# Kernel optimization log

Measured on AMD Instinct MI355X. Metric: run time of the kernel, lower is better.

## Reference

```python
import jax, jax.numpy as jnp
import numpy as np

B, L, T, H = 8, 16, 1024, 256


def setup_inputs() -> dict:
    key = jax.random.key(0)
    k1, k2 = jax.random.split(key)
    h_blth = jax.random.normal(k1, (B, L, T, H), dtype=jnp.float32)
    # nn.Linear(H, 1): weight [1, H] -> store as [H]; bias [1]
    attn_w = jax.random.normal(k2, (H,), dtype=jnp.float32) / np.sqrt(H)
    attn_b = jnp.zeros((1,), dtype=jnp.float32)
    return {"h_blth": h_blth, "attn_w": attn_w, "attn_b": attn_b}


def reference(h_blth, attn_w, attn_b):
    # scores: [B, L, T]
    s = jnp.einsum('blth,h->blt', h_blth, attn_w) + attn_b[0]
    # global max over T (matches torch .max(dim=2, keepdim=True))
    s_max = jnp.max(s, axis=2, keepdims=True)
    exp_s = jnp.exp(s - s_max)                      # [B, L, T]
    cum_exp = jnp.cumsum(exp_s, axis=2)             # [B, L, T]
    weighted_h = exp_s[..., None] * h_blth          # [B, L, T, H]
    cum_weighted_h = jnp.cumsum(weighted_h, axis=2) # [B, L, T, H]
    ctx = cum_weighted_h / (cum_exp[..., None] + 1e-12)
    return h_blth + ctx
```

## Files before the change

kernel.cpp:

```cpp
#include <hip/hip_runtime.h>


constexpr int Tn = 1024, Hn = 256;
constexpr int BL = 128;
constexpr int NCH = 8;
constexpr int CT = Tn / NCH;

__global__ __launch_bounds__(256) void k_scores(const float* __restrict__ h,
                                                const float* __restrict__ w,
                                                const float* __restrict__ bias,
                                                float* __restrict__ ebuf,
                                                float* __restrict__ P) {
    const int wave = threadIdx.x >> 6, lane = threadIdx.x & 63;
    const int chunk = blockIdx.x & 7, bl = blockIdx.x >> 3;
    const float4 w4 = reinterpret_cast<const float4*>(w)[lane];
    const float b0 = bias[0];
    const float4* hp = reinterpret_cast<const float4*>(h) + (size_t)bl * Tn * (Hn / 4);
    const int t0 = chunk * CT + wave * 32;

    float4 acc = {0.f, 0.f, 0.f, 0.f};
    #pragma unroll 4
    for (int i = 0; i < 32; ++i) {
        const int t = t0 + i;
        float4 x = hp[(size_t)t * (Hn / 4) + lane];
        float p = x.x * w4.x + x.y * w4.y + x.z * w4.z + x.w * w4.w;
        #pragma unroll
        for (int off = 32; off > 0; off >>= 1) p += __shfl_xor(p, off, 64);
        const float e = __expf(p + b0);
        acc.x = fmaf(e, x.x, acc.x);
        acc.y = fmaf(e, x.y, acc.y);
        acc.z = fmaf(e, x.z, acc.z);
        acc.w = fmaf(e, x.w, acc.w);
        if (lane == 0) ebuf[bl * Tn + t] = e;
    }

    __shared__ float4 red[4][64];
    red[wave][lane] = acc;
    __syncthreads();
    if (wave == 0) {
        float4 a = red[0][lane], b = red[1][lane], c = red[2][lane], d = red[3][lane];
        float4 s;
        s.x = (a.x + b.x) + (c.x + d.x);
        s.y = (a.y + b.y) + (c.y + d.y);
        s.z = (a.z + b.z) + (c.z + d.z);
        s.w = (a.w + b.w) + (c.w + d.w);
        reinterpret_cast<float4*>(P)[(bl * NCH + chunk) * (Hn / 4) + lane] = s;
    }
}

__global__ __launch_bounds__(256) void k_scan(const float* __restrict__ ebuf,
                                              const float* __restrict__ P,
                                              float* __restrict__ dbuf,
                                              float* __restrict__ O) {
    const int bl = blockIdx.x, tid = threadIdx.x;
    const int wave = tid >> 6, lane = tid & 63;
    __shared__ float wsum[4];

    float4 ev = reinterpret_cast<const float4*>(ebuf)[bl * (Tn / 4) + tid];
    const float tsum = ev.x + ev.y + ev.z + ev.w;
    float sc = tsum;
    #pragma unroll
    for (int off = 1; off < 64; off <<= 1) {
        float n = __shfl_up(sc, off, 64);
        if (lane >= off) sc += n;
    }
    if (lane == 63) wsum[wave] = sc;
    __syncthreads();
    float wo = 0.f;
    for (int i = 0; i < wave; ++i) wo += wsum[i];
    const float pre = wo + sc - tsum;

    const float c0 = pre + ev.x;
    const float c1 = c0 + ev.y;
    const float c2 = c1 + ev.z;
    const float c3 = c2 + ev.w;
    float4 dv;
    dv.x = 1.0f / (c0 + 1e-12f);
    dv.y = 1.0f / (c1 + 1e-12f);
    dv.z = 1.0f / (c2 + 1e-12f);
    dv.w = 1.0f / (c3 + 1e-12f);
    reinterpret_cast<float4*>(dbuf)[bl * (Tn / 4) + tid] = dv;

    float run = 0.f;
    #pragma unroll
    for (int j = 0; j < NCH; ++j) {
        O[(bl * NCH + j) * Hn + tid] = run;
        run += P[(bl * NCH + j) * Hn + tid];
    }
}

__global__ __launch_bounds__(256) void k_apply(const float* __restrict__ h,
                                               const float* __restrict__ ebuf,
                                               const float* __restrict__ dbuf,
                                               const float* __restrict__ O,
                                               float* __restrict__ out) {
    const int j = blockIdx.x & 7, bl = blockIdx.x >> 3;
    const int tid = threadIdx.x;
    __shared__ float se[CT], sd[CT];
    if (tid < CT) se[tid] = ebuf[bl * Tn + j * CT + tid];
    else          sd[tid - CT] = dbuf[bl * Tn + j * CT + (tid - CT)];
    __syncthreads();

    float acc = O[(bl * NCH + j) * Hn + tid];
    const float* hp = h   + ((size_t)bl * Tn + j * CT) * Hn + tid;
    float*       op = out + ((size_t)bl * Tn + j * CT) * Hn + tid;

    for (int t = 0; t < CT; t += 16) {
        float x[16];
        #pragma unroll
        for (int u = 0; u < 16; ++u) x[u] = hp[(size_t)(t + u) * Hn];
        #pragma unroll
        for (int u = 0; u < 16; ++u) {
            acc = fmaf(se[t + u], x[u], acc);
            op[(size_t)(t + u) * Hn] = fmaf(acc, sd[t + u], x[u]);
        }
    }
}

extern "C" void kernel_launch(void* const* d_in, const int* in_sizes, int n_in,
                              void* d_out, int out_size, void* d_ws, size_t ws_size,
                              hipStream_t stream) {
    const float* h = (const float*)d_in[0];
    const float* w = (const float*)d_in[1];
    const float* b = (const float*)d_in[2];
    float* out = (float*)d_out;

    float* ebuf = (float*)d_ws;
    float* dbuf = ebuf + BL * Tn;
    float* P    = dbuf + BL * Tn;
    float* O    = P + BL * NCH * Hn;

    k_scores<<<BL * NCH, 256, 0, stream>>>(h, w, b, ebuf, P);
    k_scan<<<BL, 256, 0, stream>>>(ebuf, P, dbuf, O);
    k_apply<<<BL * NCH, 256, 0, stream>>>(h, ebuf, dbuf, O, out);
}
```

Baseline: 259.9 us.

## Fold scan kernel into apply and process four timesteps per wave in scores

Removes the separate scan kernel. Each apply block now computes its own chunk's prefix of exp sums and running H-offset from per-chunk partial sums written by the scores kernel. The scores kernel is restructured so each wave handles four timesteps at once with 16-lane groups, which cuts the dot-product shuffle reduction from six to four steps and adds more loads in flight. The cost is redundant prefix work in each apply block plus extra cross-group shuffles at the end of the scores kernel.

```diff
diff --git a/kernel.cpp b/kernel.cpp
--- a/kernel.cpp
+++ b/kernel.cpp
@@ -5,103 +5,119 @@
 constexpr int BL = 128;
 constexpr int NCH = 8;
 constexpr int CT = Tn / NCH;
+constexpr int F4 = Hn / 4;
 
 __global__ __launch_bounds__(256) void k_scores(const float* __restrict__ h,
                                                 const float* __restrict__ w,
                                                 const float* __restrict__ bias,
                                                 float* __restrict__ ebuf,
-                                                float* __restrict__ P) {
+                                                float* __restrict__ P,
+                                                float* __restrict__ Se) {
     const int wave = threadIdx.x >> 6, lane = threadIdx.x & 63;
-    const int chunk = blockIdx.x & 7, bl = blockIdx.x >> 3;
-    const float4 w4 = reinterpret_cast<const float4*>(w)[lane];
+    const int g = lane >> 4, sub = lane & 15;
+    const int j = blockIdx.x & 7, bl = blockIdx.x >> 3;
     const float b0 = bias[0];
-    const float4* hp = reinterpret_cast<const float4*>(h) + (size_t)bl * Tn * (Hn / 4);
-    const int t0 = chunk * CT + wave * 32;
+    const float4* wp = reinterpret_cast<const float4*>(w);
+    float4 w4[4];
+    #pragma unroll
+    for (int q = 0; q < 4; ++q) w4[q] = wp[sub + 16 * q];
+    const float4* hp = reinterpret_cast<const float4*>(h) + (size_t)bl * Tn * F4;
+    const int t0 = j * CT + wave * 32;
 
-    float4 acc = {0.f, 0.f, 0.f, 0.f};
-    #pragma unroll 4
-    for (int i = 0; i < 32; ++i) {
-        const int t = t0 + i;
-        float4 x = hp[(size_t)t * (Hn / 4) + lane];
-        float p = x.x * w4.x + x.y * w4.y + x.z * w4.z + x.w * w4.w;
+    float4 acc[4] = {{0,0,0,0},{0,0,0,0},{0,0,0,0},{0,0,0,0}};
+    float esum = 0.f;
+    #pragma unroll
+    for (int i = 0; i < 8; ++i) {
+        const int t = t0 + i * 4 + g;
+        float4 x[4];
         #pragma unroll
-        for (int off = 32; off > 0; off >>= 1) p += __shfl_xor(p, off, 64);
+        for (int q = 0; q < 4; ++q) x[q] = hp[(size_t)t * F4 + sub + 16 * q];
+        float p = 0.f;
+        #pragma unroll
+        for (int q = 0; q < 4; ++q) {
+            p = fmaf(x[q].x, w4[q].x, p);
+            p = fmaf(x[q].y, w4[q].y, p);
+            p = fmaf(x[q].z, w4[q].z, p);
+            p = fmaf(x[q].w, w4[q].w, p);
+        }
+        p += __shfl_xor(p, 1, 64);
+        p += __shfl_xor(p, 2, 64);
+        p += __shfl_xor(p, 4, 64);
+        p += __shfl_xor(p, 8, 64);
         const float e = __expf(p + b0);
-        acc.x = fmaf(e, x.x, acc.x);
-        acc.y = fmaf(e, x.y, acc.y);
-        acc.z = fmaf(e, x.z, acc.z);
-        acc.w = fmaf(e, x.w, acc.w);
-        if (lane == 0) ebuf[bl * Tn + t] = e;
+        esum += e;
+        #pragma unroll
+        for (int q = 0; q < 4; ++q) {
+            acc[q].x = fmaf(e, x[q].x, acc[q].x);
+            acc[q].y = fmaf(e, x[q].y, acc[q].y);
+            acc[q].z = fmaf(e, x[q].z, acc[q].z);
+            acc[q].w = fmaf(e, x[q].w, acc[q].w);
+        }
+        if (sub == 0) ebuf[bl * Tn + t] = e;
     }
+    #pragma unroll
+    for (int q = 0; q < 4; ++q) {
+        acc[q].x += __shfl_xor(acc[q].x, 16, 64); acc[q].x += __shfl_xor(acc[q].x, 32, 64);
+        acc[q].y += __shfl_xor(acc[q].y, 16, 64); acc[q].y += __shfl_xor(acc[q].y, 32, 64);
+        acc[q].z += __shfl_xor(acc[q].z, 16, 64); acc[q].z += __shfl_xor(acc[q].z, 32, 64);
+        acc[q].w += __shfl_xor(acc[q].w, 16, 64); acc[q].w += __shfl_xor(acc[q].w, 32, 64);
+    }
+    esum += __shfl_xor(esum, 16, 64);  esum += __shfl_xor(esum, 32, 64);
 
-    __shared__ float4 red[4][64];
-    red[wave][lane] = acc;
+    __shared__ float4 redP[4][16][4];
+    __shared__ float  redS[4];
+    if (lane < 16) {
+        #pragma unroll
+        for (int q = 0; q < 4; ++q) redP[wave][lane][q] = acc[q];
+    }
+    if (lane == 0) redS[wave] = esum;
     __syncthreads();
-    if (wave == 0) {
-        float4 a = red[0][lane], b = red[1][lane], c = red[2][lane], d = red[3][lane];
+    if (threadIdx.x < 64) {
+        const int s16 = threadIdx.x & 15, q = threadIdx.x >> 4;
+        float4 a = redP[0][s16][q], b = redP[1][s16][q];
+        float4 c = redP[2][s16][q], d = redP[3][s16][q];
         float4 s;
         s.x = (a.x + b.x) + (c.x + d.x);
         s.y = (a.y + b.y) + (c.y + d.y);
         s.z = (a.z + b.z) + (c.z + d.z);
         s.w = (a.w + b.w) + (c.w + d.w);
-        reinterpret_cast<float4*>(P)[(bl * NCH + chunk) * (Hn / 4) + lane] = s;
-    }
-}
-
-__global__ __launch_bounds__(256) void k_scan(const float* __restrict__ ebuf,
-                                              const float* __restrict__ P,
-                                              float* __restrict__ dbuf,
-                                              float* __restrict__ O) {
-    const int bl = blockIdx.x, tid = threadIdx.x;
-    const int wave = tid >> 6, lane = tid & 63;
-    __shared__ float wsum[4];
-
-    float4 ev = reinterpret_cast<const float4*>(ebuf)[bl * (Tn / 4) + tid];
-    const float tsum = ev.x + ev.y + ev.z + ev.w;
-    float sc = tsum;
-    #pragma unroll
-    for (int off = 1; off < 64; off <<= 1) {
-        float n = __shfl_up(sc, off, 64);
-        if (lane >= off) sc += n;
-    }
-    if (lane == 63) wsum[wave] = sc;
-    __syncthreads();
-    float wo = 0.f;
-    for (int i = 0; i < wave; ++i) wo += wsum[i];
-    const float pre = wo + sc - tsum;
-
-    const float c0 = pre + ev.x;
-    const float c1 = c0 + ev.y;
-    const float c2 = c1 + ev.z;
-    const float c3 = c2 + ev.w;
-    float4 dv;
-    dv.x = 1.0f / (c0 + 1e-12f);
-    dv.y = 1.0f / (c1 + 1e-12f);
-    dv.z = 1.0f / (c2 + 1e-12f);
-    dv.w = 1.0f / (c3 + 1e-12f);
-    reinterpret_cast<float4*>(dbuf)[bl * (Tn / 4) + tid] = dv;
-
-    float run = 0.f;
-    #pragma unroll
-    for (int j = 0; j < NCH; ++j) {
-        O[(bl * NCH + j) * Hn + tid] = run;
-        run += P[(bl * NCH + j) * Hn + tid];
+        reinterpret_cast<float4*>(P)[(bl * NCH + j) * F4 + s16 + 16 * q] = s;
+    } else if (threadIdx.x == 64) {
+        Se[bl * NCH + j] = (redS[0] + redS[1]) + (redS[2] + redS[3]);
     }
 }
 
 __global__ __launch_bounds__(256) void k_apply(const float* __restrict__ h,
                                                const float* __restrict__ ebuf,
-                                               const float* __restrict__ dbuf,
-                                               const float* __restrict__ O,
+                                               const float* __restrict__ P,
+                                               const float* __restrict__ Se,
                                                float* __restrict__ out) {
     const int j = blockIdx.x & 7, bl = blockIdx.x >> 3;
     const int tid = threadIdx.x;
     __shared__ float se[CT], sd[CT];
     if (tid < CT) se[tid] = ebuf[bl * Tn + j * CT + tid];
-    else          sd[tid - CT] = dbuf[bl * Tn + j * CT + (tid - CT)];
     __syncthreads();
 
-    float acc = O[(bl * NCH + j) * Hn + tid];
+    if (tid < 64) {
+        float base = 0.f;
+        for (int jj = 0; jj < j; ++jj) base += Se[bl * NCH + jj];
+        float v0 = se[2 * tid], v1 = se[2 * tid + 1];
+        float ts = v0 + v1;
+        float sc = ts;
+        #pragma unroll
+        for (int off = 1; off < 64; off <<= 1) {
+            float n = __shfl_up(sc, off, 64);
+            if (tid >= off) sc += n;
+        }
+        float pre = base + sc - ts;
+        float c0 = pre + v0, c1 = c0 + v1;
+        sd[2 * tid]     = 1.0f / (c0 + 1e-12f);
+        sd[2 * tid + 1] = 1.0f / (c1 + 1e-12f);
+    }
+    float acc = 0.f;
+    for (int jj = 0; jj < j; ++jj) acc += P[(bl * NCH + jj) * Hn + tid];
+    __syncthreads();
+
     const float* hp = h   + ((size_t)bl * Tn + j * CT) * Hn + tid;
     float*       op = out + ((size_t)bl * Tn + j * CT) * Hn + tid;
 
@@ -126,11 +142,9 @@
     float* out = (float*)d_out;
 
     float* ebuf = (float*)d_ws;
-    float* dbuf = ebuf + BL * Tn;
-    float* P    = dbuf + BL * Tn;
-    float* O    = P + BL * NCH * Hn;
+    float* P    = ebuf + BL * Tn;
+    float* Se   = P + BL * NCH * Hn;
 
-    k_scores<<<BL * NCH, 256, 0, stream>>>(h, w, b, ebuf, P);
-    k_scan<<<BL, 256, 0, stream>>>(ebuf, P, dbuf, O);
-    k_apply<<<BL * NCH, 256, 0, stream>>>(h, ebuf, dbuf, O, out);
+    k_scores<<<BL * NCH, 256, 0, stream>>>(h, w, b, ebuf, P, Se);
+    k_apply<<<BL * NCH, 256, 0, stream>>>(h, ebuf, P, Se, out);
 }
```

Measured after the change: 256.9 us. About the same (-1.2%).
